# Kernel optimization log

Measured on AMD Instinct MI355X. Metric: run time of the kernel, lower is better.

The kernel has to match this reference:

```python
import jax, jax.numpy as jnp
import numpy as np

B, H, W, C = 2, 96, 192, 768
NH, HD = 12, 64
W0, W1 = 8, 8          # window size
S0, S1 = 4, 4          # shift size
N = W0 * W1
NW = (H // W0) * (W // W1)
HID = 3072             # mlp_ratio 4 * dim
SCALE = HD ** -0.5


def _ln(x, g, b):
    m = x.mean(-1, keepdims=True)
    v = ((x - m) ** 2).mean(-1, keepdims=True)
    return (x - m) * jax.lax.rsqrt(v + 1e-5) * g + b


def _partition(x):  # (B,H,W,C) -> (B*NW, W0, W1, C)
    Bb = x.shape[0]
    x = x.reshape(Bb, H // W0, W0, W // W1, W1, -1).transpose(0, 1, 3, 2, 4, 5)
    return x.reshape(-1, W0, W1, x.shape[-1])


def _reverse(w):  # (B*NW, W0, W1, C) -> (B,H,W,C)
    Cc = w.shape[-1]
    x = w.reshape(B, H // W0, W // W1, W0, W1, Cc).transpose(0, 1, 3, 2, 4, 5)
    return x.reshape(B, H, W, Cc)


def _rope2(x):  # axial 2D RoPE on (nB, W0, W1, HD): first half rotates over h, second over w
    dh = HD // 2

    def cs(L, d):
        inv = 1.0 / (10000.0 ** (jnp.arange(0, d, 2, dtype=jnp.float32) / d))
        ang = jnp.arange(L, dtype=jnp.float32)[:, None] * inv
        return jnp.cos(ang), jnp.sin(ang)

    def rot(xa, cos, sin):
        x1, x2 = xa[..., 0::2], xa[..., 1::2]
        return jnp.stack([x1 * cos - x2 * sin, x1 * sin + x2 * cos], -1).reshape(xa.shape)

    ch, sh = cs(W0, dh)
    cw, sw = cs(W1, dh)
    xh = rot(x[..., :dh], ch[:, None, :], sh[:, None, :])
    xw = rot(x[..., dh:], cw[None, :, :], sw[None, :, :])
    return jnp.concatenate([xh, xw], -1)


def _make_mask():
    # faithful port of BasicLayer.create_mask (2D path)
    img = np.zeros((H, W), np.float32)
    cnt = 0
    for hs in (slice(0, -W0), slice(-W0, -S0), slice(-S0, None)):
        for wsl in (slice(0, -W1), slice(-W1, 0), slice(0, None)):
            img[hs, wsl] = cnt
            cnt += 1
    mw = img.reshape(H // W0, W0, W // W1, W1).transpose(0, 2, 1, 3).reshape(NW, N)
    am = mw[:, None, :] - mw[:, :, None]
    return jnp.asarray(np.where(am != 0, -100.0, 0.0).astype(np.float32))


def setup_inputs():
    key = jax.random.key(0)
    ks = jax.random.split(key, 6)
    s = lambda k, shape, fan: jax.random.normal(k, shape, jnp.float32) * (fan ** -0.5)
    return dict(
        x=jax.random.normal(ks[0], (B, H * W, C), jnp.float32),
        mask=_make_mask(),
        w_qkv=s(ks[1], (3 * C, C), C), b_qkv=jnp.zeros((3 * C,), jnp.float32),
        w_proj=s(ks[2], (C, C), C), b_proj=jnp.zeros((C,), jnp.float32),
        g1=jnp.ones((C,), jnp.float32), b1=jnp.zeros((C,), jnp.float32),
        g2=jnp.ones((C,), jnp.float32), b2=jnp.zeros((C,), jnp.float32),
        w_fc1=s(ks[3], (HID, C), C), b_fc1=jnp.zeros((HID,), jnp.float32),
        w_fc2=s(ks[4], (C, HID), HID), b_fc2=jnp.zeros((C,), jnp.float32),
    )


def reference(x, mask, w_qkv, b_qkv, w_proj, b_proj, g1, b1, g2, b2,
              w_fc1, b_fc1, w_fc2, b_fc2):
    shortcut = x
    xi = x.reshape(B, H, W, C)
    xi = jnp.roll(xi, (-S0, -S1), axis=(1, 2))
    xw = _partition(xi).reshape(-1, N, C)  # (B*NW, N, C)
    B_ = xw.shape[0]
    qkv = (xw @ w_qkv.T + b_qkv).reshape(B_, N, 3, NH, HD).transpose(2, 0, 3, 1, 4)
    q, k, v = qkv[0], qkv[1], qkv[2]  # (B_, NH, N, HD)
    q = _rope2(q.reshape(-1, W0, W1, HD)).reshape(B_, NH, N, HD)
    k = _rope2(k.reshape(-1, W0, W1, HD)).reshape(B_, NH, N, HD)
    attn = jnp.einsum('bhnd,bhmd->bhnm', q * SCALE, k)
    attn = attn.reshape(B, NW, NH, N, N) + mask[None, :, None]
    attn = jax.nn.softmax(attn.reshape(B_, NH, N, N), axis=-1)
    out = jnp.einsum('bhnm,bhmd->bnhd', attn, v).reshape(B_, N, C)
    out = out @ w_proj.T + b_proj
    xr = _reverse(out.reshape(-1, W0, W1, C))
    xr = jnp.roll(xr, (S0, S1), axis=(1, 2)).reshape(B, H * W, C)
    x1 = _ln(shortcut + xr, g1, b1)          # post-norm residual, as in source
    h = jax.nn.relu(x1 @ w_fc1.T + b_fc1) @ w_fc2.T + b_fc2
    return _ln(x1 + h, g2, b2)
```

## Files before the change

### kernel.cpp

```cpp
#include <hip/hip_runtime.h>
#include <math.h>
#include <stddef.h>

#define NTOK   36864
#define CDIM   768
#define HIDDIM 3072
#define QKVDIM 2304

typedef unsigned short u16;
typedef unsigned int   u32;
typedef __attribute__((ext_vector_type(8))) short short8;
typedef __attribute__((ext_vector_type(4))) short short4v;
typedef __attribute__((ext_vector_type(4))) float f32x4;

__device__ __forceinline__ float bf2f(u16 h) { return __uint_as_float(((u32)h) << 16); }
__device__ __forceinline__ u16 f2bf(float f) {
  u32 u = __float_as_uint(f);
  u32 r = u + 0x7fffu + ((u >> 16) & 1u);
  return (u16)(r >> 16);
}

__device__ __forceinline__ int win_row_to_src(int r) {
  int n = r & 63;
  int wflat = r >> 6;
  int b = wflat / 288;
  int wi = wflat - b * 288;
  int wh = wi / 24;
  int ww = wi - wh * 24;
  int i0 = n >> 3, i1 = n & 7;
  int hh = wh * 8 + i0 + 4; if (hh >= 96)  hh -= 96;
  int wp = ww * 8 + i1 + 4; if (wp >= 192) wp -= 192;
  return b * 18432 + hh * 192 + wp;
}

__device__ __forceinline__ void load_lds16(const u16* g, u16* l) {
  __builtin_amdgcn_global_load_lds((const __attribute__((address_space(1))) void*)g,
                                   (__attribute__((address_space(3))) void*)l, 16, 0, 0);
}

template<int OUTBF, int RELU, int RES>
__launch_bounds__(256, 2)
__global__ void gemm128(const u16* __restrict__ A, const u16* __restrict__ Wt,
                        const float* __restrict__ bias, const u16* __restrict__ res,
                        void* __restrict__ Cout, int M, int N, int K,
                        int gridx, int nwg)
{
  const int orig = blockIdx.x;
  const int xcd  = orig & 7;
  const int q    = nwg >> 3, r8 = nwg & 7;
  const int wgid = (xcd < r8 ? xcd * (q + 1) : r8 * (q + 1) + (xcd - r8) * q) + (orig >> 3);
  int bn, bm;
  if (((gridx | nwg) & 1) == 0) {
    const int halfn = nwg >> 1, hc = gridx >> 1;
    const int half  = (wgid >= halfn) ? 1 : 0;
    const int w2    = wgid - half * halfn;
    bn = (w2 % hc + half * hc) * 128;
    bm = (w2 / hc) * 128;
  } else {
    bn = (wgid % gridx) * 128;
    bm = (wgid / gridx) * 128;
  }

  __shared__ __align__(16) u16 lds[2][2][128 * 64];

  const int t    = threadIdx.x;
  const int wv   = t >> 6, lane = t & 63;
  const int wm   = wv >> 1, wn = wv & 1;
  const int lr   = lane & 15, lg = lane >> 4;
  const int sr   = t >> 3;
  const int ss   = t & 7;

  const u16* Abase = A  + (size_t)bm * K;
  const u16* Bbase = Wt + (size_t)bn * K;

  const int nt = K >> 6;

  auto stage = [&](int kt, int b) {
    const int k0 = kt << 6;
#pragma unroll
    for (int j = 0; j < 4; j++) {
      int row  = j * 32 + sr;
      int slot = ss ^ (row & 7);
      load_lds16(Abase + (size_t)row * K + k0 + slot * 8, &lds[b][0][j * 2048 + t * 8]);
    }
#pragma unroll
    for (int j = 0; j < 4; j++) {
      int row  = j * 32 + sr;
      int slot = ss ^ (row & 7);
      load_lds16(Bbase + (size_t)row * K + k0 + slot * 8, &lds[b][1][j * 2048 + t * 8]);
    }
  };

  f32x4 acc[4][4] = {};

  stage(0, 0);
  stage(1, 1);

  for (int tt = 0; tt < nt; tt++) {
    const int cur = tt & 1;
    if (tt + 1 < nt) asm volatile("s_waitcnt vmcnt(8)" ::: "memory");
    else             asm volatile("s_waitcnt vmcnt(0)" ::: "memory");
    __builtin_amdgcn_s_barrier();

    const u16* Ab = &lds[cur][0][0];
    const u16* Bb = &lds[cur][1][0];

    short8 bfr[4][2], afr[4][2];
#pragma unroll
    for (int nf = 0; nf < 4; nf++)
#pragma unroll
      for (int ks = 0; ks < 2; ks++) {
        int row = wn * 64 + nf * 16 + lr;
        bfr[nf][ks] = *(const short8*)(Bb + row * 64 + (((ks * 4 + lg) ^ (row & 7)) << 3));
      }
#pragma unroll
    for (int mf = 0; mf < 4; mf++)
#pragma unroll
      for (int ks = 0; ks < 2; ks++) {
        int row = wm * 64 + mf * 16 + lr;
        afr[mf][ks] = *(const short8*)(Ab + row * 64 + (((ks * 4 + lg) ^ (row & 7)) << 3));
      }
    asm volatile("s_waitcnt lgkmcnt(0)" ::: "memory");
    __builtin_amdgcn_sched_barrier(0);

    __builtin_amdgcn_s_setprio(1);
#pragma unroll
    for (int mf = 0; mf < 4; mf++)
#pragma unroll
      for (int nf = 0; nf < 4; nf++)
        acc[mf][nf] = __builtin_amdgcn_mfma_f32_16x16x32_bf16(bfr[nf][0], afr[mf][0], acc[mf][nf], 0, 0, 0);
    __builtin_amdgcn_s_setprio(0);

    __builtin_amdgcn_s_barrier();

    if (tt + 2 < nt) stage(tt + 2, cur);

    __builtin_amdgcn_s_setprio(1);
#pragma unroll
    for (int mf = 0; mf < 4; mf++)
#pragma unroll
      for (int nf = 0; nf < 4; nf++)
        acc[mf][nf] = __builtin_amdgcn_mfma_f32_16x16x32_bf16(bfr[nf][1], afr[mf][1], acc[mf][nf], 0, 0, 0);
    __builtin_amdgcn_s_setprio(0);
  }

#pragma unroll
  for (int mf = 0; mf < 4; mf++) {
    size_t row = (size_t)(bm + wm * 64 + mf * 16 + lr);
#pragma unroll
    for (int nf = 0; nf < 4; nf++) {
      int col0 = bn + wn * 64 + nf * 16 + lg * 4;
      float4 b4 = *(const float4*)(bias + col0);
      float v0 = acc[mf][nf][0] + b4.x;
      float v1 = acc[mf][nf][1] + b4.y;
      float v2 = acc[mf][nf][2] + b4.z;
      float v3 = acc[mf][nf][3] + b4.w;
      if (RELU) {
        v0 = fmaxf(v0, 0.f); v1 = fmaxf(v1, 0.f);
        v2 = fmaxf(v2, 0.f); v3 = fmaxf(v3, 0.f);
      }
      if (RES) {
        short4v rv = *(const short4v*)(res + row * N + col0);
        v0 += bf2f((u16)rv[0]); v1 += bf2f((u16)rv[1]);
        v2 += bf2f((u16)rv[2]); v3 += bf2f((u16)rv[3]);
      }
      if (OUTBF) {
        short4v o;
        o[0] = (short)f2bf(v0); o[1] = (short)f2bf(v1);
        o[2] = (short)f2bf(v2); o[3] = (short)f2bf(v3);
        *(short4v*)((u16*)Cout + row * N + col0) = o;
      } else {
        f32x4 o = {v0, v1, v2, v3};
        *(f32x4*)((float*)Cout + row * N + col0) = o;
      }
    }
  }
}

__launch_bounds__(256)
__global__ void gather_x_bf16(const float* __restrict__ x, u16* __restrict__ xg)
{
  const int t = threadIdx.x, wv = t >> 6, lane = t & 63;
  const int r = blockIdx.x * 4 + wv;
  const float4* src = (const float4*)(x + (size_t)win_row_to_src(r) * CDIM);
  short4v* dst = (short4v*)(xg + (size_t)r * CDIM);
#pragma unroll
  for (int e = 0; e < 3; e++) {
    float4 f = src[e * 64 + lane];
    short4v o;
    o[0] = (short)f2bf(f.x); o[1] = (short)f2bf(f.y);
    o[2] = (short)f2bf(f.z); o[3] = (short)f2bf(f.w);
    dst[e * 64 + lane] = o;
  }
}

__launch_bounds__(256)
__global__ void conv_bf16(const float* __restrict__ in, u16* __restrict__ out, int n)
{
  int i = blockIdx.x * 256 + threadIdx.x;
  if (i < n) out[i] = f2bf(in[i]);
}

__launch_bounds__(256)
__global__ void attn_mfma(const u16* __restrict__ qkv, const float* __restrict__ mask,
                          u16* __restrict__ out)
{
  __shared__ u16 vt[4][4096];
  __shared__ u16 pbuf[4][4096];
  __shared__ float ropetab[512];

  const int t = threadIdx.x;
  {
    int p = t >> 3, pos = t & 7;
    float inv = __expf(-(float)(p & 15) * 0.5756462732485115f);
    float sv, cv;
    sincosf((float)pos * inv, &sv, &cv);
    ropetab[t * 2]     = cv;
    ropetab[t * 2 + 1] = sv;
  }
  __syncthreads();

  const int wv = t >> 6, lane = t & 63;
  const int lr = lane & 15, lg = lane >> 4;
  const int gp   = blockIdx.x * 4 + wv;
  const int head = gp % 12;
  const int lw   = gp / 12;
  const int widx = lw % 288;
  const u16* base = qkv + (size_t)lw * 64 * QKVDIM + head * 64;

  {
    const u16* vrow = base + 1536 + (size_t)lane * QKVDIM;
    u16* vb = vt[wv];
#pragma unroll
    for (int s = 0; s < 8; s++) {
      short8 v = *(const short8*)(vrow + s * 8);
#pragma unroll
      for (int j = 0; j < 8; j++) {
        int d = s * 8 + j;
        vb[d * 64 + ((((lane >> 3) ^ (d & 7)) << 3) | (lane & 7))] = (u16)v[j];
      }
    }
  }

  short8 aq[4][2], ak[4][2];
#pragma unroll
  for (int f = 0; f < 4; f++) {
#pragma unroll
    for (int ks = 0; ks < 2; ks++) {
      int n = f * 16 + lr;
      short8 qv = *(const short8*)(base + (size_t)n * QKVDIM + ks * 32 + lg * 8);
      short8 kv = *(const short8*)(base + (size_t)n * QKVDIM + 768 + ks * 32 + lg * 8);
      short8 qo, ko;
#pragma unroll
      for (int jj = 0; jj < 4; jj++) {
        int p   = ks * 16 + lg * 4 + jj;
        int pos = (p < 16) ? (n >> 3) : (n & 7);
        float cv = ropetab[(p * 8 + pos) * 2];
        float sv = ropetab[(p * 8 + pos) * 2 + 1];
        float q1 = bf2f((u16)qv[2 * jj]), q2 = bf2f((u16)qv[2 * jj + 1]);
        float k1 = bf2f((u16)kv[2 * jj]), k2 = bf2f((u16)kv[2 * jj + 1]);
        qo[2 * jj]     = (short)f2bf((q1 * cv - q2 * sv) * 0.125f);
        qo[2 * jj + 1] = (short)f2bf((q1 * sv + q2 * cv) * 0.125f);
        ko[2 * jj]     = (short)f2bf(k1 * cv - k2 * sv);
        ko[2 * jj + 1] = (short)f2bf(k1 * sv + k2 * cv);
      }
      aq[f][ks] = qo; ak[f][ks] = ko;
    }
  }

  f32x4 sf[4][4] = {};
#pragma unroll
  for (int ks = 0; ks < 2; ks++)
#pragma unroll
    for (int fn = 0; fn < 4; fn++)
#pragma unroll
      for (int fm = 0; fm < 4; fm++)
        sf[fn][fm] = __builtin_amdgcn_mfma_f32_16x16x32_bf16(aq[fn][ks], ak[fm][ks], sf[fn][fm], 0, 0, 0);

  const float* mrow = mask + (size_t)widx * 4096;
#pragma unroll
  for (int fn = 0; fn < 4; fn++)
#pragma unroll
    for (int fm = 0; fm < 4; fm++)
#pragma unroll
      for (int j = 0; j < 4; j++)
        sf[fn][fm][j] += mrow[(fn * 16 + lg * 4 + j) * 64 + fm * 16 + lr];

#pragma unroll
  for (int fn = 0; fn < 4; fn++) {
#pragma unroll
    for (int j = 0; j < 4; j++) {
      float m0 = fmaxf(fmaxf(sf[fn][0][j], sf[fn][1][j]),
                       fmaxf(sf[fn][2][j], sf[fn][3][j]));
      m0 = fmaxf(m0, __shfl_xor(m0, 1));
      m0 = fmaxf(m0, __shfl_xor(m0, 2));
      m0 = fmaxf(m0, __shfl_xor(m0, 4));
      m0 = fmaxf(m0, __shfl_xor(m0, 8));
      float s0 = 0.f;
#pragma unroll
      for (int fm = 0; fm < 4; fm++) {
        float e = __expf(sf[fn][fm][j] - m0);
        sf[fn][fm][j] = e;
        s0 += e;
      }
      s0 += __shfl_xor(s0, 1);
      s0 += __shfl_xor(s0, 2);
      s0 += __shfl_xor(s0, 4);
      s0 += __shfl_xor(s0, 8);
      float r = 1.f / s0;
#pragma unroll
      for (int fm = 0; fm < 4; fm++) sf[fn][fm][j] *= r;
    }
  }

  u16* pb = pbuf[wv];
#pragma unroll
  for (int fn = 0; fn < 4; fn++)
#pragma unroll
    for (int fm = 0; fm < 4; fm++)
#pragma unroll
      for (int j = 0; j < 4; j++) {
        int n = fn * 16 + lg * 4 + j, m = fm * 16 + lr;
        pb[n * 64 + ((((m >> 3) ^ (n & 7)) << 3) | (m & 7))] = f2bf(sf[fn][fm][j]);
      }
  asm volatile("s_waitcnt lgkmcnt(0)" ::: "memory");
  __builtin_amdgcn_sched_barrier(0);

  short8 ap[4][2], bvf[4][2];
#pragma unroll
  for (int f = 0; f < 4; f++)
#pragma unroll
    for (int ks = 0; ks < 2; ks++) {
      int rn = f * 16 + lr;
      ap[f][ks]  = *(const short8*)(pb     + rn * 64 + (((ks * 4 + lg) ^ (rn & 7)) << 3));
      bvf[f][ks] = *(const short8*)(vt[wv] + rn * 64 + (((ks * 4 + lg) ^ (rn & 7)) << 3));
    }
  f32x4 o[4][4] = {};
#pragma unroll
  for (int ks = 0; ks < 2; ks++)
#pragma unroll
    for (int fn = 0; fn < 4; fn++)
#pragma unroll
      for (int fd = 0; fd < 4; fd++)
        o[fn][fd] = __builtin_amdgcn_mfma_f32_16x16x32_bf16(bvf[fd][ks], ap[fn][ks], o[fn][fd], 0, 0, 0);

  u16* ob = out + ((size_t)lw * 64) * CDIM + head * 64;
#pragma unroll
  for (int fn = 0; fn < 4; fn++) {
    size_t nrow = (size_t)(fn * 16 + lr) * CDIM;
#pragma unroll
    for (int fd = 0; fd < 4; fd++) {
      int d0 = fd * 16 + lg * 4;
      short4v ov;
      ov[0] = (short)f2bf(o[fn][fd][0]);
      ov[1] = (short)f2bf(o[fn][fd][1]);
      ov[2] = (short)f2bf(o[fn][fd][2]);
      ov[3] = (short)f2bf(o[fn][fd][3]);
      *(short4v*)(ob + nrow + d0) = ov;
    }
  }
}

__launch_bounds__(256)
__global__ void ln1_kernel(const float* __restrict__ xin, const u16* __restrict__ add,
                           const float* __restrict__ g, const float* __restrict__ bb,
                           u16* __restrict__ out)
{
  const int t = threadIdx.x, wv = t >> 6, lane = t & 63;
  const int tok = blockIdx.x * 4 + wv;
  int b = tok / 18432;
  int hw = tok - b * 18432;
  int h = hw / 192, w = hw - h * 192;
  int h2 = h - 4; if (h2 < 0) h2 += 96;
  int w2 = w - 4; if (w2 < 0) w2 += 192;
  int r = ((b * 12 + (h2 >> 3)) * 24 + (w2 >> 3)) * 64 + (h2 & 7) * 8 + (w2 & 7);
  const float4*  a0 = (const float4*)(xin + (size_t)tok * CDIM);
  const short4v* a1 = (const short4v*)(add + (size_t)r * CDIM);

  float v[12];
  float s1 = 0.f, s2 = 0.f;
#pragma unroll
  for (int e = 0; e < 3; e++) {
    float4  f = a0[e * 64 + lane];
    short4v a = a1[e * 64 + lane];
    float x0 = f.x + bf2f((u16)a[0]);
    float x1 = f.y + bf2f((u16)a[1]);
    float x2 = f.z + bf2f((u16)a[2]);
    float x3 = f.w + bf2f((u16)a[3]);
    v[e*4+0] = x0; v[e*4+1] = x1; v[e*4+2] = x2; v[e*4+3] = x3;
    s1 += x0 + x1 + x2 + x3;
    s2 += x0*x0 + x1*x1 + x2*x2 + x3*x3;
  }
#pragma unroll
  for (int m = 1; m < 64; m <<= 1) {
    s1 += __shfl_xor(s1, m);
    s2 += __shfl_xor(s2, m);
  }
  float mean = s1 * (1.f / 768.f);
  float var  = s2 * (1.f / 768.f) - mean * mean;
  float rs   = rsqrtf(var + 1e-5f);
  short4v* dst = (short4v*)(out + (size_t)tok * CDIM);
#pragma unroll
  for (int e = 0; e < 3; e++) {
    short4v o;
#pragma unroll
    for (int j = 0; j < 4; j++) {
      int c = (e * 64 + lane) * 4 + j;
      o[j] = (short)f2bf((v[e*4+j] - mean) * rs * g[c] + bb[c]);
    }
    dst[e * 64 + lane] = o;
  }
}

__launch_bounds__(256)
__global__ void ln2_kernel(const u16* __restrict__ xin, const float* __restrict__ g,
                           const float* __restrict__ bb, float* __restrict__ out)
{
  const int t = threadIdx.x, wv = t >> 6, lane = t & 63;
  const int tok = blockIdx.x * 4 + wv;
  const short4v* a0 = (const short4v*)(xin + (size_t)tok * CDIM);

  float v[12];
  float s1 = 0.f, s2 = 0.f;
#pragma unroll
  for (int e = 0; e < 3; e++) {
    short4v a = a0[e * 64 + lane];
#pragma unroll
    for (int j = 0; j < 4; j++) {
      float x = bf2f((u16)a[j]);
      v[e*4+j] = x; s1 += x; s2 += x * x;
    }
  }
#pragma unroll
  for (int m = 1; m < 64; m <<= 1) {
    s1 += __shfl_xor(s1, m);
    s2 += __shfl_xor(s2, m);
  }
  float mean = s1 * (1.f / 768.f);
  float var  = s2 * (1.f / 768.f) - mean * mean;
  float rs   = rsqrtf(var + 1e-5f);
  float4* dst = (float4*)(out + (size_t)tok * CDIM);
#pragma unroll
  for (int e = 0; e < 3; e++) {
    float4 o;
    int c = (e * 64 + lane) * 4;
    o.x = (v[e*4+0] - mean) * rs * g[c+0] + bb[c+0];
    o.y = (v[e*4+1] - mean) * rs * g[c+1] + bb[c+1];
    o.z = (v[e*4+2] - mean) * rs * g[c+2] + bb[c+2];
    o.w = (v[e*4+3] - mean) * rs * g[c+3] + bb[c+3];
    dst[e * 64 + lane] = o;
  }
}

static inline void launch_gemm(const u16* A, const u16* Wt, const float* bias,
                               const u16* res, void* C, int M, int N, int K,
                               int outbf, int relu, int resf, hipStream_t s)
{
  int gridx = N / 128, nwg = gridx * (M / 128);
  if (outbf) {
    if (relu)      gemm128<1,1,0><<<nwg, 256, 0, s>>>(A, Wt, bias, res, C, M, N, K, gridx, nwg);
    else if (resf) gemm128<1,0,1><<<nwg, 256, 0, s>>>(A, Wt, bias, res, C, M, N, K, gridx, nwg);
    else           gemm128<1,0,0><<<nwg, 256, 0, s>>>(A, Wt, bias, res, C, M, N, K, gridx, nwg);
  } else {
    gemm128<0,0,0><<<nwg, 256, 0, s>>>(A, Wt, bias, res, C, M, N, K, gridx, nwg);
  }
}

extern "C" void kernel_launch(void* const* d_in, const int* in_sizes, int n_in,
                              void* d_out, int out_size, void* d_ws, size_t ws_size,
                              hipStream_t stream)
{
  const float* x      = (const float*)d_in[0];
  const float* mask   = (const float*)d_in[1];
  const float* w_qkv  = (const float*)d_in[2];
  const float* b_qkv  = (const float*)d_in[3];
  const float* w_proj = (const float*)d_in[4];
  const float* b_proj = (const float*)d_in[5];
  const float* g1     = (const float*)d_in[6];
  const float* b1     = (const float*)d_in[7];
  const float* g2     = (const float*)d_in[8];
  const float* b2     = (const float*)d_in[9];
  const float* w_fc1  = (const float*)d_in[10];
  const float* b_fc1  = (const float*)d_in[11];
  const float* w_fc2  = (const float*)d_in[12];
  const float* b_fc2  = (const float*)d_in[13];
  float* out = (float*)d_out;

  char* base = (char*)d_ws;
  u16* P1  = (u16*)base;
  u16* QKV = (u16*)(base + 56623104);
  u16* Hb  = QKV;
  u16* Yb  = (u16*)(base + 56623104 + 113246208);
  u16* P3  = (u16*)(base + 56623104 + 169869312);
  u16* wqkvb  = (u16*)(base + 56623104 + 169869312 + 56623104);
  u16* wprojb = wqkvb  + 1769472;
  u16* wfc1b  = wprojb + 589824;
  u16* wfc2b  = wfc1b  + 2359296;

  conv_bf16<<<(1769472 + 255) / 256, 256, 0, stream>>>(w_qkv,  wqkvb,  1769472);
  conv_bf16<<<( 589824 + 255) / 256, 256, 0, stream>>>(w_proj, wprojb,  589824);
  conv_bf16<<<(2359296 + 255) / 256, 256, 0, stream>>>(w_fc1,  wfc1b,  2359296);
  conv_bf16<<<(2359296 + 255) / 256, 256, 0, stream>>>(w_fc2,  wfc2b,  2359296);
  gather_x_bf16<<<NTOK / 4, 256, 0, stream>>>(x, P1);

  launch_gemm(P1, wqkvb, b_qkv, nullptr, QKV, NTOK, QKVDIM, CDIM, 1, 0, 0, stream);
  attn_mfma<<<576 * 12 / 4, 256, 0, stream>>>(QKV, mask, P1);

  launch_gemm(P1, wprojb, b_proj, nullptr, P3, NTOK, CDIM, CDIM, 1, 0, 0, stream);

  ln1_kernel<<<NTOK / 4, 256, 0, stream>>>(x, P3, g1, b1, P1);

  for (int c = 0; c < 2; c++) {
    const u16* x1c = P1 + (size_t)c * 18432 * CDIM;
    launch_gemm(x1c, wfc1b, b_fc1, nullptr, Hb, 18432, HIDDIM, CDIM, 1, 1, 0, stream);
    launch_gemm(Hb, wfc2b, b_fc2, x1c, Yb + (size_t)c * 18432 * CDIM,
                18432, CDIM, HIDDIM, 1, 0, 1, stream);
  }

  ln2_kernel<<<NTOK / 4, 256, 0, stream>>>(Yb, g2, b2, out);
}
```

Baseline: 888.1 us.

## Use 8-wave GEMM tiles, bf16 residual in LN1, and unchunked MLP

The 128x128 GEMM now runs 512 threads as 2x4 waves, each owning a 64x32 sub-tile. The A fragments are loaded in two halves around the barrier and the stage issues fewer loads per thread, with the vmcnt wait adjusted to match. The aim is more waves to hide latency and fewer registers per wave. LN1 now reads the gathered bf16 copy of x instead of fp32 x, which cuts its read bandwidth but rounds the residual to bf16. The MLP runs as one fc1/fc2 pair over all tokens, with fc2 writing its residual output in place, on a workspace layout rebuilt to fit the larger hidden buffer.

```diff
diff --git a/kernel.cpp b/kernel.cpp
--- a/kernel.cpp
+++ b/kernel.cpp
@@ -39,7 +39,7 @@
 }
 
 template<int OUTBF, int RELU, int RES>
-__launch_bounds__(256, 2)
+__launch_bounds__(512, 4)
 __global__ void gemm128(const u16* __restrict__ A, const u16* __restrict__ Wt,
                         const float* __restrict__ bias, const u16* __restrict__ res,
                         void* __restrict__ Cout, int M, int N, int K,
@@ -65,7 +65,7 @@
 
   const int t    = threadIdx.x;
   const int wv   = t >> 6, lane = t & 63;
-  const int wm   = wv >> 1, wn = wv & 1;
+  const int wm   = wv >> 2, wn = wv & 3;
   const int lr   = lane & 15, lg = lane >> 4;
   const int sr   = t >> 3;
   const int ss   = t & 7;
@@ -78,43 +78,43 @@
   auto stage = [&](int kt, int b) {
     const int k0 = kt << 6;
 #pragma unroll
-    for (int j = 0; j < 4; j++) {
-      int row  = j * 32 + sr;
+    for (int j = 0; j < 2; j++) {
+      int row  = j * 64 + sr;
       int slot = ss ^ (row & 7);
-      load_lds16(Abase + (size_t)row * K + k0 + slot * 8, &lds[b][0][j * 2048 + t * 8]);
-    }
-#pragma unroll
-    for (int j = 0; j < 4; j++) {
-      int row  = j * 32 + sr;
+      load_lds16(Abase + (size_t)row * K + k0 + slot * 8, &lds[b][0][j * 4096 + t * 8]);
+    }
+#pragma unroll
+    for (int j = 0; j < 2; j++) {
+      int row  = j * 64 + sr;
       int slot = ss ^ (row & 7);
-      load_lds16(Bbase + (size_t)row * K + k0 + slot * 8, &lds[b][1][j * 2048 + t * 8]);
+      load_lds16(Bbase + (size_t)row * K + k0 + slot * 8, &lds[b][1][j * 4096 + t * 8]);
     }
   };
 
-  f32x4 acc[4][4] = {};
+  f32x4 acc[4][2] = {};
 
   stage(0, 0);
   stage(1, 1);
 
   for (int tt = 0; tt < nt; tt++) {
     const int cur = tt & 1;
-    if (tt + 1 < nt) asm volatile("s_waitcnt vmcnt(8)" ::: "memory");
+    if (tt + 1 < nt) asm volatile("s_waitcnt vmcnt(4)" ::: "memory");
     else             asm volatile("s_waitcnt vmcnt(0)" ::: "memory");
     __builtin_amdgcn_s_barrier();
 
     const u16* Ab = &lds[cur][0][0];
     const u16* Bb = &lds[cur][1][0];
 
-    short8 bfr[4][2], afr[4][2];
-#pragma unroll
-    for (int nf = 0; nf < 4; nf++)
+    short8 bfr[2][2], afr[2][2];
+#pragma unroll
+    for (int nf = 0; nf < 2; nf++)
 #pragma unroll
       for (int ks = 0; ks < 2; ks++) {
-        int row = wn * 64 + nf * 16 + lr;
+        int row = wn * 32 + nf * 16 + lr;
         bfr[nf][ks] = *(const short8*)(Bb + row * 64 + (((ks * 4 + lg) ^ (row & 7)) << 3));
       }
 #pragma unroll
-    for (int mf = 0; mf < 4; mf++)
+    for (int mf = 0; mf < 2; mf++)
 #pragma unroll
       for (int ks = 0; ks < 2; ks++) {
         int row = wm * 64 + mf * 16 + lr;
@@ -122,25 +122,38 @@
       }
     asm volatile("s_waitcnt lgkmcnt(0)" ::: "memory");
     __builtin_amdgcn_sched_barrier(0);
-
     __builtin_amdgcn_s_setprio(1);
 #pragma unroll
-    for (int mf = 0; mf < 4; mf++)
-#pragma unroll
-      for (int nf = 0; nf < 4; nf++)
-        acc[mf][nf] = __builtin_amdgcn_mfma_f32_16x16x32_bf16(bfr[nf][0], afr[mf][0], acc[mf][nf], 0, 0, 0);
+    for (int ks = 0; ks < 2; ks++)
+#pragma unroll
+      for (int mf = 0; mf < 2; mf++)
+#pragma unroll
+        for (int nf = 0; nf < 2; nf++)
+          acc[mf][nf] = __builtin_amdgcn_mfma_f32_16x16x32_bf16(bfr[nf][ks], afr[mf][ks], acc[mf][nf], 0, 0, 0);
     __builtin_amdgcn_s_setprio(0);
 
+    short8 afr2[2][2];
+#pragma unroll
+    for (int mf = 0; mf < 2; mf++)
+#pragma unroll
+      for (int ks = 0; ks < 2; ks++) {
+        int row = wm * 64 + (mf + 2) * 16 + lr;
+        afr2[mf][ks] = *(const short8*)(Ab + row * 64 + (((ks * 4 + lg) ^ (row & 7)) << 3));
+      }
+    asm volatile("s_waitcnt lgkmcnt(0)" ::: "memory");
+    __builtin_amdgcn_sched_barrier(0);
     __builtin_amdgcn_s_barrier();
 
     if (tt + 2 < nt) stage(tt + 2, cur);
 
     __builtin_amdgcn_s_setprio(1);
 #pragma unroll
-    for (int mf = 0; mf < 4; mf++)
-#pragma unroll
-      for (int nf = 0; nf < 4; nf++)
-        acc[mf][nf] = __builtin_amdgcn_mfma_f32_16x16x32_bf16(bfr[nf][1], afr[mf][1], acc[mf][nf], 0, 0, 0);
+    for (int ks = 0; ks < 2; ks++)
+#pragma unroll
+      for (int mf = 0; mf < 2; mf++)
+#pragma unroll
+        for (int nf = 0; nf < 2; nf++)
+          acc[mf + 2][nf] = __builtin_amdgcn_mfma_f32_16x16x32_bf16(bfr[nf][ks], afr2[mf][ks], acc[mf + 2][nf], 0, 0, 0);
     __builtin_amdgcn_s_setprio(0);
   }
 
@@ -148,8 +161,8 @@
   for (int mf = 0; mf < 4; mf++) {
     size_t row = (size_t)(bm + wm * 64 + mf * 16 + lr);
 #pragma unroll
-    for (int nf = 0; nf < 4; nf++) {
-      int col0 = bn + wn * 64 + nf * 16 + lg * 4;
+    for (int nf = 0; nf < 2; nf++) {
+      int col0 = bn + wn * 32 + nf * 16 + lg * 4;
       float4 b4 = *(const float4*)(bias + col0);
       float v0 = acc[mf][nf][0] + b4.x;
       float v1 = acc[mf][nf][1] + b4.y;
@@ -362,7 +375,7 @@
 }
 
 __launch_bounds__(256)
-__global__ void ln1_kernel(const float* __restrict__ xin, const u16* __restrict__ add,
+__global__ void ln1_kernel(const u16* __restrict__ xg, const u16* __restrict__ add,
                            const float* __restrict__ g, const float* __restrict__ bb,
                            u16* __restrict__ out)
 {
@@ -374,22 +387,20 @@
   int h2 = h - 4; if (h2 < 0) h2 += 96;
   int w2 = w - 4; if (w2 < 0) w2 += 192;
   int r = ((b * 12 + (h2 >> 3)) * 24 + (w2 >> 3)) * 64 + (h2 & 7) * 8 + (w2 & 7);
-  const float4*  a0 = (const float4*)(xin + (size_t)tok * CDIM);
+  const short4v* a0 = (const short4v*)(xg  + (size_t)r * CDIM);
   const short4v* a1 = (const short4v*)(add + (size_t)r * CDIM);
 
   float v[12];
   float s1 = 0.f, s2 = 0.f;
 #pragma unroll
   for (int e = 0; e < 3; e++) {
-    float4  f = a0[e * 64 + lane];
+    short4v f = a0[e * 64 + lane];
     short4v a = a1[e * 64 + lane];
-    float x0 = f.x + bf2f((u16)a[0]);
-    float x1 = f.y + bf2f((u16)a[1]);
-    float x2 = f.z + bf2f((u16)a[2]);
-    float x3 = f.w + bf2f((u16)a[3]);
-    v[e*4+0] = x0; v[e*4+1] = x1; v[e*4+2] = x2; v[e*4+3] = x3;
-    s1 += x0 + x1 + x2 + x3;
-    s2 += x0*x0 + x1*x1 + x2*x2 + x3*x3;
+#pragma unroll
+    for (int j = 0; j < 4; j++) {
+      float x = bf2f((u16)f[j]) + bf2f((u16)a[j]);
+      v[e*4+j] = x; s1 += x; s2 += x * x;
+    }
   }
 #pragma unroll
   for (int m = 1; m < 64; m <<= 1) {
@@ -458,11 +469,11 @@
 {
   int gridx = N / 128, nwg = gridx * (M / 128);
   if (outbf) {
-    if (relu)      gemm128<1,1,0><<<nwg, 256, 0, s>>>(A, Wt, bias, res, C, M, N, K, gridx, nwg);
-    else if (resf) gemm128<1,0,1><<<nwg, 256, 0, s>>>(A, Wt, bias, res, C, M, N, K, gridx, nwg);
-    else           gemm128<1,0,0><<<nwg, 256, 0, s>>>(A, Wt, bias, res, C, M, N, K, gridx, nwg);
+    if (relu)      gemm128<1,1,0><<<nwg, 512, 0, s>>>(A, Wt, bias, res, C, M, N, K, gridx, nwg);
+    else if (resf) gemm128<1,0,1><<<nwg, 512, 0, s>>>(A, Wt, bias, res, C, M, N, K, gridx, nwg);
+    else           gemm128<1,0,0><<<nwg, 512, 0, s>>>(A, Wt, bias, res, C, M, N, K, gridx, nwg);
   } else {
-    gemm128<0,0,0><<<nwg, 256, 0, s>>>(A, Wt, bias, res, C, M, N, K, gridx, nwg);
+    gemm128<0,0,0><<<nwg, 512, 0, s>>>(A, Wt, bias, res, C, M, N, K, gridx, nwg);
   }
 }
 
@@ -487,12 +498,11 @@
   float* out = (float*)d_out;
 
   char* base = (char*)d_ws;
-  u16* P1  = (u16*)base;
-  u16* QKV = (u16*)(base + 56623104);
-  u16* Hb  = QKV;
-  u16* Yb  = (u16*)(base + 56623104 + 113246208);
-  u16* P3  = (u16*)(base + 56623104 + 169869312);
-  u16* wqkvb  = (u16*)(base + 56623104 + 169869312 + 56623104);
+  u16* A0 = (u16*)base;
+  u16* A1 = (u16*)(base + 56623104);
+  u16* A2 = (u16*)(base + 226492416);
+  u16* Hb = (u16*)base;
+  u16* wqkvb  = (u16*)(base + 283115520);
   u16* wprojb = wqkvb  + 1769472;
   u16* wfc1b  = wprojb + 589824;
   u16* wfc2b  = wfc1b  + 2359296;
@@ -501,21 +511,17 @@
   conv_bf16<<<( 589824 + 255) / 256, 256, 0, stream>>>(w_proj, wprojb,  589824);
   conv_bf16<<<(2359296 + 255) / 256, 256, 0, stream>>>(w_fc1,  wfc1b,  2359296);
   conv_bf16<<<(2359296 + 255) / 256, 256, 0, stream>>>(w_fc2,  wfc2b,  2359296);
-  gather_x_bf16<<<NTOK / 4, 256, 0, stream>>>(x, P1);
-
-  launch_gemm(P1, wqkvb, b_qkv, nullptr, QKV, NTOK, QKVDIM, CDIM, 1, 0, 0, stream);
-  attn_mfma<<<576 * 12 / 4, 256, 0, stream>>>(QKV, mask, P1);
-
-  launch_gemm(P1, wprojb, b_proj, nullptr, P3, NTOK, CDIM, CDIM, 1, 0, 0, stream);
-
-  ln1_kernel<<<NTOK / 4, 256, 0, stream>>>(x, P3, g1, b1, P1);
-
-  for (int c = 0; c < 2; c++) {
-    const u16* x1c = P1 + (size_t)c * 18432 * CDIM;
-    launch_gemm(x1c, wfc1b, b_fc1, nullptr, Hb, 18432, HIDDIM, CDIM, 1, 1, 0, stream);
-    launch_gemm(Hb, wfc2b, b_fc2, x1c, Yb + (size_t)c * 18432 * CDIM,
-                18432, CDIM, HIDDIM, 1, 0, 1, stream);
-  }
-
-  ln2_kernel<<<NTOK / 4, 256, 0, stream>>>(Yb, g2, b2, out);
-}
+  gather_x_bf16<<<NTOK / 4, 256, 0, stream>>>(x, A0);
+
+  launch_gemm(A0, wqkvb, b_qkv, nullptr, A1, NTOK, QKVDIM, CDIM, 1, 0, 0, stream);
+  attn_mfma<<<576 * 12 / 4, 256, 0, stream>>>(A1, mask, A2);
+
+  launch_gemm(A2, wprojb, b_proj, nullptr, A1, NTOK, CDIM, CDIM, 1, 0, 0, stream);
+
+  ln1_kernel<<<NTOK / 4, 256, 0, stream>>>(A0, A1, g1, b1, A2);
+
+  launch_gemm(A2, wfc1b, b_fc1, nullptr, Hb, NTOK, HIDDIM, CDIM, 1, 1, 0, stream);
+  launch_gemm(Hb, wfc2b, b_fc2, A2, A2, NTOK, CDIM, HIDDIM, 1, 0, 1, stream);
+
+  ln2_kernel<<<NTOK / 4, 256, 0, stream>>>(A2, g2, b2, out);
+}
```

New measurement: 866.2 us. 1.03x faster.
